# Kernel tuning notes

Measured on AMD Instinct MI355X. Metric: run time of the kernel, lower is better.

## Reference

```python
import jax, jax.numpy as jnp
import numpy as np

K, N, MEM_D = 512, 4096, 64


def setup_inputs() -> dict:
    key = jax.random.key(0)
    k1, k2, k3, k4 = jax.random.split(key, 4)
    # event counts per location/time (torch code uses raw observations; rand in [0,1) keeps log-lik finite)
    obs = jax.random.uniform(k1, (K, N), jnp.float32)
    extobs = jax.random.normal(k2, (K, N), jnp.float32)
    beta = jnp.asarray(2.0, jnp.float32)  # torch.Tensor([2]) scalar rate parameter
    alpha = jax.random.uniform(k3, (K, K), jnp.float32, 0.0, 0.01)
    gamma = jax.random.uniform(k4, (K, MEM_D), jnp.float32, 0.0, 0.01)
    return {"obs": obs, "extobs": extobs, "beta": beta, "alpha": alpha, "gamma": gamma}


def reference(obs, extobs, beta, alpha, gamma):
    Kk, Nn = obs.shape
    d = gamma.shape[1]
    # mu is derived from obs exactly as in __init__ (not a trainable parameter)
    mu = obs.mean(axis=1) / 10.0 + 0.01  # [K]

    t = jnp.arange(Nn)
    diff = t[:, None] - t[None, :]  # [N, N], diff[t, j] = t - j
    # strict lower-triangular exponential decay kernel: D[t, j] = beta * exp(-(t-j)*beta) for j < t
    # clamp diff before exp so masked entries never produce inf (keeps vjp NaN-free)
    safe = jnp.maximum(diff, 1).astype(jnp.float32)
    Dmat = jnp.where(diff > 0, beta * jnp.exp(-safe * beta), 0.0)  # [N, N]

    # lam1[k, t] = sum_{k'} alpha[k, k'] * sum_{j < t} obs[k', j] * beta * exp(-(t-j)*beta)
    lam1 = alpha @ (obs @ Dmat.T)  # [K, N]

    # lam2[k, t] = sum_i extobs[k, t-d+i] * gamma[k, i]  (only when t >= d, else 0)
    # depthwise 1D cross-correlation with left zero-padding of d, then mask t < d
    x = extobs[None]            # [1, K, N]
    w = gamma[:, None, :]       # [K, 1, d]
    lam2 = jax.lax.conv_general_dilated(
        x, w, window_strides=(1,), padding=[(d, 0)],
        dimension_numbers=("NCH", "OIH", "NCH"), feature_group_count=Kk,
    )[0, :, :Nn]                # [K, N]
    lam2 = jnp.where(t[None, :] >= d, lam2, 0.0)

    lams = jax.nn.softplus(mu[:, None] + lam1 + lam2)  # [K, N]
    loglik = (obs * jnp.log(lams) - lams).sum()
    return (loglik, lams)
```

## Files before the change

kernel.cpp:

```cpp
#include <hip/hip_runtime.h>
#include <math.h>

#define KDIM 512
#define NDIM 4096
#define MEMD 64
#define WTAPS 16

typedef short bf16x8 __attribute__((ext_vector_type(8)));
typedef float f32x4 __attribute__((ext_vector_type(4)));

__device__ __forceinline__ void bsplit(float a, ushort& hi, ushort& lo) {
    uint u = __float_as_uint(a);
    uint h = (u + 0x7FFFu + ((u >> 16) & 1u)) >> 16;
    hi = (ushort)h;
    float hf = __uint_as_float(h << 16);
    float r = a - hf;
    uint u2 = __float_as_uint(r);
    lo = (ushort)((u2 + 0x7FFFu + ((u2 >> 16) & 1u)) >> 16);
}

__device__ __forceinline__ float block_reduce_256(float v, float* sbuf) {
    #pragma unroll
    for (int off = 32; off > 0; off >>= 1) v += __shfl_down(v, off, 64);
    int lane = threadIdx.x & 63, wid = threadIdx.x >> 6;
    if (lane == 0) sbuf[wid] = v;
    __syncthreads();
    float tot = sbuf[0] + sbuf[1] + sbuf[2] + sbuf[3];
    __syncthreads();
    return tot;
}

__device__ __forceinline__ double block_reduce_256d(double v, double* dbuf) {
    #pragma unroll
    for (int off = 32; off > 0; off >>= 1) v += __shfl_down(v, off, 64);
    int lane = threadIdx.x & 63, wid = threadIdx.x >> 6;
    if (lane == 0) dbuf[wid] = v;
    __syncthreads();
    double tot = dbuf[0] + dbuf[1] + dbuf[2] + dbuf[3];
    __syncthreads();
    return tot;
}

__global__ __launch_bounds__(256) void convA(const float* __restrict__ A,
                                             ushort* __restrict__ Ahi,
                                             ushort* __restrict__ Alo) {
    int g = blockIdx.x * 256 + threadIdx.x;
    const float4* src = (const float4*)A;
    #pragma unroll
    for (int i = 0; i < 2; ++i) {
        float4 v = src[g * 2 + i];
        ushort4 h, l;
        bsplit(v.x, h.x, l.x); bsplit(v.y, h.y, l.y);
        bsplit(v.z, h.z, l.z); bsplit(v.w, h.w, l.w);
        *(ushort4*)&Ahi[(size_t)g * 8 + i * 4] = h;
        *(ushort4*)&Alo[(size_t)g * 8 + i * 4] = l;
    }
}

__global__ __launch_bounds__(256) void convB(const float* __restrict__ B,
                                             ushort* __restrict__ Bthi,
                                             ushort* __restrict__ Btlo) {
    __shared__ float s[32][33];
    int n0 = blockIdx.x * 32, k0 = blockIdx.y * 32;
    int tid = threadIdx.x;
    int r = tid >> 5, c = tid & 31;
    #pragma unroll
    for (int i = 0; i < 4; ++i)
        s[r + i * 8][c] = B[(size_t)(k0 + r + i * 8) * NDIM + n0 + c];
    __syncthreads();
    int rr = tid >> 4, cc = (tid & 15) * 2;
    #pragma unroll
    for (int i = 0; i < 2; ++i) {
        int n = rr + i * 16;
        float a0 = s[cc][n], a1 = s[cc + 1][n];
        ushort h0, l0, h1, l1;
        bsplit(a0, h0, l0); bsplit(a1, h1, l1);
        size_t o = (size_t)(n0 + n) * KDIM + k0 + cc;
        *(ushort2*)&Bthi[o] = make_ushort2(h0, h1);
        *(ushort2*)&Btlo[o] = make_ushort2(l0, l1);
    }
}

#define GBM 64
#define GBN 64
#define GBK 64

__global__ __launch_bounds__(256) void mfma_gemm(
    const ushort* __restrict__ Ahi, const ushort* __restrict__ Alo,
    const ushort* __restrict__ Bthi, const ushort* __restrict__ Btlo,
    float* __restrict__ C) {
    __shared__ __align__(16) ushort Asm[2][GBM * GBK];
    __shared__ __align__(16) ushort Bsm[2][GBN * GBK];
    int tid = threadIdx.x;
    int m0 = blockIdx.y * GBM, n0 = blockIdx.x * GBN;
    int l = tid & 63, w = tid >> 6;
    int wm = w >> 1, wn = w & 1;
    int lr = l & 15, lk = l >> 4;

    f32x4 acc[2][2];
    #pragma unroll
    for (int i = 0; i < 2; ++i)
        #pragma unroll
        for (int j = 0; j < 2; ++j) acc[i][j] = (f32x4){0.f, 0.f, 0.f, 0.f};

    for (int c0 = 0; c0 < KDIM; c0 += GBK) {
        #pragma unroll
        for (int i = 0; i < 4; ++i) {
            int c = tid + i * 256;
            int plane = c >> 9;
            int row = (c >> 3) & 63;
            int kc = c & 7;
            int off = row * 128 + ((kc * 16) ^ ((row & 7) << 4));
            const ushort* sa = (plane ? Alo : Ahi) + (size_t)(m0 + row) * KDIM + c0 + kc * 8;
            *(uint4*)((char*)&Asm[plane][0] + off) = *(const uint4*)sa;
            const ushort* sb = (plane ? Btlo : Bthi) + (size_t)(n0 + row) * KDIM + c0 + kc * 8;
            *(uint4*)((char*)&Bsm[plane][0] + off) = *(const uint4*)sb;
        }
        __syncthreads();
        bf16x8 ah[2][2], al[2][2], bh[2][2], bl[2][2];
        #pragma unroll
        for (int mf = 0; mf < 2; ++mf)
            #pragma unroll
            for (int s = 0; s < 2; ++s) {
                int ra = wm * 32 + mf * 16 + lr;
                int offa = ra * 128 + (((s * 64) + lk * 16) ^ ((ra & 7) << 4));
                ah[mf][s] = *(const bf16x8*)((const char*)&Asm[0][0] + offa);
                al[mf][s] = *(const bf16x8*)((const char*)&Asm[1][0] + offa);
                int rb = wn * 32 + mf * 16 + lr;
                int offb = rb * 128 + (((s * 64) + lk * 16) ^ ((rb & 7) << 4));
                bh[mf][s] = *(const bf16x8*)((const char*)&Bsm[0][0] + offb);
                bl[mf][s] = *(const bf16x8*)((const char*)&Bsm[1][0] + offb);
            }
        #pragma unroll
        for (int s = 0; s < 2; ++s)
            #pragma unroll
            for (int mf = 0; mf < 2; ++mf)
                #pragma unroll
                for (int nf = 0; nf < 2; ++nf) {
                    acc[mf][nf] = __builtin_amdgcn_mfma_f32_16x16x32_bf16(ah[mf][s], bh[nf][s], acc[mf][nf], 0, 0, 0);
                    acc[mf][nf] = __builtin_amdgcn_mfma_f32_16x16x32_bf16(ah[mf][s], bl[nf][s], acc[mf][nf], 0, 0, 0);
                    acc[mf][nf] = __builtin_amdgcn_mfma_f32_16x16x32_bf16(al[mf][s], bh[nf][s], acc[mf][nf], 0, 0, 0);
                }
        __syncthreads();
    }
    #pragma unroll
    for (int mf = 0; mf < 2; ++mf)
        #pragma unroll
        for (int nf = 0; nf < 2; ++nf)
            #pragma unroll
            for (int j = 0; j < 4; ++j) {
                int rm = m0 + wm * 32 + mf * 16 + lk * 4 + j;
                int cn = n0 + wn * 32 + nf * 16 + lr;
                C[(size_t)rm * NDIM + cn] = acc[mf][nf][j];
            }
}

__device__ __forceinline__ int chunk_off(int cch) {
    return ((cch & ~7) | ((cch ^ (cch >> 3)) & 7)) * 16;
}
__device__ __forceinline__ float4 lds_chunk(const float* buf, int cch) {
    return *(const float4*)((const char*)buf + chunk_off(cch));
}
__device__ __forceinline__ void lds_chunk_store(float* buf, int cch, float4 v) {
    *(float4*)((char*)buf + chunk_off(cch)) = v;
}

__global__ __launch_bounds__(256) void final_kernel(
    const float* __restrict__ T, const float* __restrict__ obs,
    const float* __restrict__ extobs, const float* __restrict__ gamma,
    const float* __restrict__ beta_p,
    float* __restrict__ lams_out, double* __restrict__ partials) {
    __shared__ float Trow[NDIM];
    __shared__ float Erow[NDIM];
    __shared__ float sbuf[4];
    __shared__ double dbuf[4];

    int k = blockIdx.x, tid = threadIdx.x;
    float beta = *beta_p;

    const float4* t4 = (const float4*)(T + (size_t)k * NDIM);
    const float4* e4 = (const float4*)(extobs + (size_t)k * NDIM);
    const float4* o4 = (const float4*)(obs + (size_t)k * NDIM);

    #pragma unroll
    for (int i = 0; i < 4; ++i) {
        int c = tid + i * 256;
        lds_chunk_store(Trow, c, t4[c]);
        lds_chunk_store(Erow, c, e4[c]);
    }
    float ov[16];
    float osum = 0.f;
    #pragma unroll
    for (int i = 0; i < 4; ++i) {
        float4 o = o4[tid * 4 + i];
        ov[i * 4 + 0] = o.x; ov[i * 4 + 1] = o.y;
        ov[i * 4 + 2] = o.z; ov[i * 4 + 3] = o.w;
        osum += (o.x + o.y) + (o.z + o.w);
    }
    float wtap[WTAPS];
    #pragma unroll
    for (int m = 0; m < WTAPS; ++m) wtap[m] = beta * expf(-beta * (float)(m + 1));

    float mu;
    {
        float tot = block_reduce_256(osum, sbuf);
        mu = tot / (float)NDIM / 10.0f + 0.01f;
    }

    float l2[16];
    #pragma unroll
    for (int j = 0; j < 16; ++j) l2[j] = 0.f;
    const float* gk = gamma + (size_t)k * MEMD;
    if (tid >= 4) {
        float wnd[80];
        int cb = tid * 4 - 16;
        #pragma unroll
        for (int c = 0; c < 20; ++c) *(float4*)&wnd[c * 4] = lds_chunk(Erow, cb + c);
        #pragma unroll
        for (int i = 0; i < MEMD; ++i) {
            float g = gk[i];
            #pragma unroll
            for (int j = 0; j < 16; ++j) l2[j] = fmaf(g, wnd[i + j], l2[j]);
        }
    }

    float l1[16];
    #pragma unroll
    for (int j = 0; j < 16; ++j) l1[j] = 0.f;
    {
        float v[WTAPS + 16];
        int cb = tid * 4 - WTAPS / 4;
        #pragma unroll
        for (int c = 0; c < (WTAPS + 16) / 4; ++c) {
            int idx = cb + c;
            float4 x = (idx >= 0) ? lds_chunk(Trow, idx) : make_float4(0.f, 0.f, 0.f, 0.f);
            *(float4*)&v[c * 4] = x;
        }
        #pragma unroll
        for (int m = 1; m <= WTAPS; ++m) {
            float wm = wtap[m - 1];
            #pragma unroll
            for (int j = 0; j < 16; ++j) l1[j] = fmaf(wm, v[WTAPS + j - m], l1[j]);
        }
    }

    float* lrp = lams_out + (size_t)k * NDIM;
    double part = 0.0;
    int t0 = tid * 16;
    #pragma unroll
    for (int i = 0; i < 4; ++i) {
        f32x4 sv;
        #pragma unroll
        for (int q = 0; q < 4; ++q) {
            int j = i * 4 + q;
            float x = mu + l1[j] + l2[j];
            float sp = fmaxf(x, 0.f) + log1pf(expf(-fabsf(x)));
            sv[q] = sp;
            part += (double)(ov[j] * logf(sp) - sp);
        }
        *(f32x4*)&lrp[t0 + i * 4] = sv;
    }
    double dtot = block_reduce_256d(part, dbuf);
    if (tid == 0) partials[k] = dtot;
}

__global__ __launch_bounds__(256) void reduce_kernel(const double* __restrict__ partials,
                                                     float* __restrict__ out) {
    __shared__ double dbuf[4];
    double v = 0.0;
    for (int j = threadIdx.x; j < KDIM; j += 256) v += partials[j];
    double tot = block_reduce_256d(v, dbuf);
    if (threadIdx.x == 0) out[0] = (float)tot;
}

extern "C" void kernel_launch(void* const* d_in, const int* in_sizes, int n_in,
                              void* d_out, int out_size, void* d_ws, size_t ws_size,
                              hipStream_t stream) {
    const float* obs    = (const float*)d_in[0];
    const float* extobs = (const float*)d_in[1];
    const float* beta   = (const float*)d_in[2];
    const float* alpha  = (const float*)d_in[3];
    const float* gamma  = (const float*)d_in[4];
    float* out = (float*)d_out;

    char* ws = (char*)d_ws;
    float*  T        = (float*)(ws);
    ushort* Bthi     = (ushort*)(ws + (8u << 20));
    ushort* Btlo     = (ushort*)(ws + (12u << 20));
    ushort* Ahi      = (ushort*)(ws + (16u << 20));
    ushort* Alo      = (ushort*)(ws + (16u << 20) + (512u << 10));
    double* partials = (double*)(ws + (17u << 20));

    convA<<<KDIM * KDIM / (256 * 8), 256, 0, stream>>>(alpha, Ahi, Alo);
    convB<<<dim3(NDIM / 32, KDIM / 32), 256, 0, stream>>>(obs, Bthi, Btlo);
    mfma_gemm<<<dim3(NDIM / GBN, KDIM / GBM), 256, 0, stream>>>(Ahi, Alo, Bthi, Btlo, T);
    final_kernel<<<KDIM, 256, 0, stream>>>(T, obs, extobs, gamma, beta, out + 1, partials);
    reduce_kernel<<<1, 256, 0, stream>>>(partials, out);
}
```

Measured before the change: 109.5 us.

## Merge conversion kernels, fold reduction via atomic counter, use direct global-to-LDS loads

Merges the alpha and obs bf16 split kernels into one launch. Removes the separate reduce kernel: the last final_kernel block, found through an atomic counter, sums the partials. The GEMM tile load now uses global_load_lds to write directly into LDS, with the swizzle moved to the source address. The final kernel also stages obs and gamma in LDS and restructures the depthwise conv into chunked windows to reduce register pressure, which adds LDS usage and may lower occupancy.

```diff
diff --git a/kernel.cpp b/kernel.cpp
--- a/kernel.cpp
+++ b/kernel.cpp
@@ -6,8 +6,16 @@
 #define MEMD 64
 #define WTAPS 16
 
+#define GBM 64
+#define GBN 64
+#define GBK 64
+
 typedef short bf16x8 __attribute__((ext_vector_type(8)));
 typedef float f32x4 __attribute__((ext_vector_type(4)));
+
+#define GLOAD_LDS16(g, l) __builtin_amdgcn_global_load_lds( \
+    (const __attribute__((address_space(1))) unsigned int*)(g), \
+    (__attribute__((address_space(3))) unsigned int*)(l), 16, 0, 0)
 
 __device__ __forceinline__ void bsplit(float a, ushort& hi, ushort& lo) {
     uint u = __float_as_uint(a);
@@ -41,49 +49,47 @@
     return tot;
 }
 
-__global__ __launch_bounds__(256) void convA(const float* __restrict__ A,
-                                             ushort* __restrict__ Ahi,
-                                             ushort* __restrict__ Alo) {
-    int g = blockIdx.x * 256 + threadIdx.x;
-    const float4* src = (const float4*)A;
-    #pragma unroll
-    for (int i = 0; i < 2; ++i) {
-        float4 v = src[g * 2 + i];
-        ushort4 h, l;
-        bsplit(v.x, h.x, l.x); bsplit(v.y, h.y, l.y);
-        bsplit(v.z, h.z, l.z); bsplit(v.w, h.w, l.w);
-        *(ushort4*)&Ahi[(size_t)g * 8 + i * 4] = h;
-        *(ushort4*)&Alo[(size_t)g * 8 + i * 4] = l;
-    }
-}
-
-__global__ __launch_bounds__(256) void convB(const float* __restrict__ B,
-                                             ushort* __restrict__ Bthi,
-                                             ushort* __restrict__ Btlo) {
+__global__ __launch_bounds__(256) void conv_kernel(
+    const float* __restrict__ B, const float* __restrict__ A,
+    ushort* __restrict__ Bthi, ushort* __restrict__ Btlo,
+    ushort* __restrict__ Ahi, ushort* __restrict__ Alo,
+    unsigned int* __restrict__ cnt) {
     __shared__ float s[32][33];
-    int n0 = blockIdx.x * 32, k0 = blockIdx.y * 32;
-    int tid = threadIdx.x;
-    int r = tid >> 5, c = tid & 31;
-    #pragma unroll
-    for (int i = 0; i < 4; ++i)
-        s[r + i * 8][c] = B[(size_t)(k0 + r + i * 8) * NDIM + n0 + c];
-    __syncthreads();
-    int rr = tid >> 4, cc = (tid & 15) * 2;
-    #pragma unroll
-    for (int i = 0; i < 2; ++i) {
-        int n = rr + i * 16;
-        float a0 = s[cc][n], a1 = s[cc + 1][n];
-        ushort h0, l0, h1, l1;
-        bsplit(a0, h0, l0); bsplit(a1, h1, l1);
-        size_t o = (size_t)(n0 + n) * KDIM + k0 + cc;
-        *(ushort2*)&Bthi[o] = make_ushort2(h0, h1);
-        *(ushort2*)&Btlo[o] = make_ushort2(l0, l1);
-    }
-}
-
-#define GBM 64
-#define GBN 64
-#define GBK 64
+    int b = blockIdx.x, tid = threadIdx.x;
+    if (b < 2048) {
+        int n0 = (b & 127) * 32, k0 = (b >> 7) * 32;
+        int r = tid >> 5, c = tid & 31;
+        #pragma unroll
+        for (int i = 0; i < 4; ++i)
+            s[r + i * 8][c] = B[(size_t)(k0 + r + i * 8) * NDIM + n0 + c];
+        __syncthreads();
+        int rr = tid >> 4, cc = (tid & 15) * 2;
+        #pragma unroll
+        for (int i = 0; i < 2; ++i) {
+            int n = rr + i * 16;
+            float a0 = s[cc][n], a1 = s[cc + 1][n];
+            ushort h0, l0, h1, l1;
+            bsplit(a0, h0, l0); bsplit(a1, h1, l1);
+            size_t o = (size_t)(n0 + n) * KDIM + k0 + cc;
+            *(ushort2*)&Bthi[o] = make_ushort2(h0, h1);
+            *(ushort2*)&Btlo[o] = make_ushort2(l0, l1);
+        }
+    } else {
+        int ab = b - 2048;
+        if (ab == 0 && tid == 0) *cnt = 0u;
+        int g = ab * 256 + tid;
+        const float4* src = (const float4*)A;
+        #pragma unroll
+        for (int i = 0; i < 2; ++i) {
+            float4 v = src[g * 2 + i];
+            ushort4 h, l;
+            bsplit(v.x, h.x, l.x); bsplit(v.y, h.y, l.y);
+            bsplit(v.z, h.z, l.z); bsplit(v.w, h.w, l.w);
+            *(ushort4*)&Ahi[(size_t)g * 8 + i * 4] = h;
+            *(ushort4*)&Alo[(size_t)g * 8 + i * 4] = l;
+        }
+    }
+}
 
 __global__ __launch_bounds__(256) void mfma_gemm(
     const ushort* __restrict__ Ahi, const ushort* __restrict__ Alo,
@@ -107,14 +113,12 @@
         #pragma unroll
         for (int i = 0; i < 4; ++i) {
             int c = tid + i * 256;
-            int plane = c >> 9;
-            int row = (c >> 3) & 63;
-            int kc = c & 7;
-            int off = row * 128 + ((kc * 16) ^ ((row & 7) << 4));
+            int plane = c >> 9, q = c & 511;
+            int row = q >> 3, kc = (q & 7) ^ (row & 7);
             const ushort* sa = (plane ? Alo : Ahi) + (size_t)(m0 + row) * KDIM + c0 + kc * 8;
-            *(uint4*)((char*)&Asm[plane][0] + off) = *(const uint4*)sa;
+            GLOAD_LDS16(sa, (char*)&Asm[0][0] + c * 16);
             const ushort* sb = (plane ? Btlo : Bthi) + (size_t)(n0 + row) * KDIM + c0 + kc * 8;
-            *(uint4*)((char*)&Bsm[plane][0] + off) = *(const uint4*)sb;
+            GLOAD_LDS16(sb, (char*)&Bsm[0][0] + c * 16);
         }
         __syncthreads();
         bf16x8 ah[2][2], al[2][2], bh[2][2], bl[2][2];
@@ -169,11 +173,15 @@
     const float* __restrict__ T, const float* __restrict__ obs,
     const float* __restrict__ extobs, const float* __restrict__ gamma,
     const float* __restrict__ beta_p,
-    float* __restrict__ lams_out, double* __restrict__ partials) {
+    float* __restrict__ lams_out, double* __restrict__ partials,
+    unsigned int* __restrict__ cnt, float* __restrict__ loglik_out) {
     __shared__ float Trow[NDIM];
     __shared__ float Erow[NDIM];
+    __shared__ float Orow[NDIM];
+    __shared__ float Grow[MEMD];
     __shared__ float sbuf[4];
     __shared__ double dbuf[4];
+    __shared__ unsigned int flagS;
 
     int k = blockIdx.x, tid = threadIdx.x;
     float beta = *beta_p;
@@ -182,21 +190,18 @@
     const float4* e4 = (const float4*)(extobs + (size_t)k * NDIM);
     const float4* o4 = (const float4*)(obs + (size_t)k * NDIM);
 
+    float osum = 0.f;
     #pragma unroll
     for (int i = 0; i < 4; ++i) {
         int c = tid + i * 256;
         lds_chunk_store(Trow, c, t4[c]);
         lds_chunk_store(Erow, c, e4[c]);
-    }
-    float ov[16];
-    float osum = 0.f;
-    #pragma unroll
-    for (int i = 0; i < 4; ++i) {
-        float4 o = o4[tid * 4 + i];
-        ov[i * 4 + 0] = o.x; ov[i * 4 + 1] = o.y;
-        ov[i * 4 + 2] = o.z; ov[i * 4 + 3] = o.w;
+        float4 o = o4[c];
+        lds_chunk_store(Orow, c, o);
         osum += (o.x + o.y) + (o.z + o.w);
     }
+    if (tid < MEMD) Grow[tid] = gamma[(size_t)k * MEMD + tid];
+
     float wtap[WTAPS];
     #pragma unroll
     for (int m = 0; m < WTAPS; ++m) wtap[m] = beta * expf(-beta * (float)(m + 1));
@@ -207,48 +212,54 @@
         mu = tot / (float)NDIM / 10.0f + 0.01f;
     }
 
-    float l2[16];
-    #pragma unroll
-    for (int j = 0; j < 16; ++j) l2[j] = 0.f;
-    const float* gk = gamma + (size_t)k * MEMD;
-    if (tid >= 4) {
-        float wnd[80];
-        int cb = tid * 4 - 16;
-        #pragma unroll
-        for (int c = 0; c < 20; ++c) *(float4*)&wnd[c * 4] = lds_chunk(Erow, cb + c);
-        #pragma unroll
-        for (int i = 0; i < MEMD; ++i) {
-            float g = gk[i];
-            #pragma unroll
-            for (int j = 0; j < 16; ++j) l2[j] = fmaf(g, wnd[i + j], l2[j]);
-        }
-    }
+    int t0 = tid * 16;
 
     float l1[16];
     #pragma unroll
     for (int j = 0; j < 16; ++j) l1[j] = 0.f;
     {
-        float v[WTAPS + 16];
-        int cb = tid * 4 - WTAPS / 4;
-        #pragma unroll
-        for (int c = 0; c < (WTAPS + 16) / 4; ++c) {
+        float win[32];
+        int cb = tid * 4 - 4;
+        #pragma unroll
+        for (int c = 0; c < 8; ++c) {
             int idx = cb + c;
             float4 x = (idx >= 0) ? lds_chunk(Trow, idx) : make_float4(0.f, 0.f, 0.f, 0.f);
-            *(float4*)&v[c * 4] = x;
+            *(float4*)&win[c * 4] = x;
         }
         #pragma unroll
         for (int m = 1; m <= WTAPS; ++m) {
             float wm = wtap[m - 1];
             #pragma unroll
-            for (int j = 0; j < 16; ++j) l1[j] = fmaf(wm, v[WTAPS + j - m], l1[j]);
+            for (int j = 0; j < 16; ++j) l1[j] = fmaf(wm, win[16 + j - m], l1[j]);
+        }
+    }
+
+    float l2[16];
+    #pragma unroll
+    for (int j = 0; j < 16; ++j) l2[j] = 0.f;
+    if (tid >= 4) {
+        #pragma unroll
+        for (int c4 = 0; c4 < 4; ++c4) {
+            float win[32];
+            int cb = tid * 4 - 16 + c4 * 4;
+            #pragma unroll
+            for (int c = 0; c < 8; ++c)
+                *(float4*)&win[c * 4] = lds_chunk(Erow, cb + c);
+            #pragma unroll
+            for (int i = 0; i < 16; ++i) {
+                float g = Grow[c4 * 16 + i];
+                #pragma unroll
+                for (int j = 0; j < 16; ++j) l2[j] = fmaf(g, win[i + j], l2[j]);
+            }
         }
     }
 
     float* lrp = lams_out + (size_t)k * NDIM;
     double part = 0.0;
-    int t0 = tid * 16;
     #pragma unroll
     for (int i = 0; i < 4; ++i) {
+        float4 o = lds_chunk(Orow, tid * 4 + i);
+        float oo[4] = {o.x, o.y, o.z, o.w};
         f32x4 sv;
         #pragma unroll
         for (int q = 0; q < 4; ++q) {
@@ -256,21 +267,25 @@
             float x = mu + l1[j] + l2[j];
             float sp = fmaxf(x, 0.f) + log1pf(expf(-fabsf(x)));
             sv[q] = sp;
-            part += (double)(ov[j] * logf(sp) - sp);
+            part += (double)(oo[q] * logf(sp) - sp);
         }
         *(f32x4*)&lrp[t0 + i * 4] = sv;
     }
     double dtot = block_reduce_256d(part, dbuf);
-    if (tid == 0) partials[k] = dtot;
-}
-
-__global__ __launch_bounds__(256) void reduce_kernel(const double* __restrict__ partials,
-                                                     float* __restrict__ out) {
-    __shared__ double dbuf[4];
-    double v = 0.0;
-    for (int j = threadIdx.x; j < KDIM; j += 256) v += partials[j];
-    double tot = block_reduce_256d(v, dbuf);
-    if (threadIdx.x == 0) out[0] = (float)tot;
+    if (tid == 0) {
+        partials[k] = dtot;
+        __threadfence();
+        unsigned int old = atomicAdd(cnt, 1u);
+        flagS = (old == (unsigned int)(KDIM - 1)) ? 1u : 0u;
+    }
+    __syncthreads();
+    if (flagS) {
+        __threadfence();
+        double v = 0.0;
+        for (int j = tid; j < KDIM; j += 256) v += partials[j];
+        double tot = block_reduce_256d(v, dbuf);
+        if (tid == 0) loglik_out[0] = (float)tot;
+    }
 }
 
 extern "C" void kernel_launch(void* const* d_in, const int* in_sizes, int n_in,
@@ -290,10 +305,10 @@
     ushort* Ahi      = (ushort*)(ws + (16u << 20));
     ushort* Alo      = (ushort*)(ws + (16u << 20) + (512u << 10));
     double* partials = (double*)(ws + (17u << 20));
-
-    convA<<<KDIM * KDIM / (256 * 8), 256, 0, stream>>>(alpha, Ahi, Alo);
-    convB<<<dim3(NDIM / 32, KDIM / 32), 256, 0, stream>>>(obs, Bthi, Btlo);
+    unsigned int* cnt = (unsigned int*)(ws + (17u << 20) + 4096);
+
+    conv_kernel<<<2048 + 128, 256, 0, stream>>>(obs, alpha, Bthi, Btlo, Ahi, Alo, cnt);
     mfma_gemm<<<dim3(NDIM / GBN, KDIM / GBM), 256, 0, stream>>>(Ahi, Alo, Bthi, Btlo, T);
-    final_kernel<<<KDIM, 256, 0, stream>>>(T, obs, extobs, gamma, beta, out + 1, partials);
-    reduce_kernel<<<1, 256, 0, stream>>>(partials, out);
-}
+    final_kernel<<<KDIM, 256, 0, stream>>>(T, obs, extobs, gamma, beta,
+                                           out + 1, partials, cnt, out);
+}
```

After: 121.1 us. 1.11x slower.
